# Kernel optimization log

Hardware: AMD Instinct MI355X
Metric: run time of the kernel (lower is better)

The kernel has to match this reference:

```python
import jax, jax.numpy as jnp
import numpy as np

IN_FEATURES = 4096
OUT_FEATURES = 4096
MIN_PREC = 3   # min(precisions)
MAXMEM = 6
BL, BH = 4, 5  # floor/ceil of p = sigmoid(0)*3 + 3 = 4.5 (static, matches p.item() usage)


def dequant_kbit(qweight, lut, b):
    """Bitplane LUT dequant: qweight (P, O, IN//32) int32, lut (O, 2**b) -> (O, IN) float.
    Plane j holds one bit per weight (32 weights packed per int32, LSB-first within
    the int32); the first b planes form the b-bit code, plane 0 being the MSB."""
    planes = qweight[:b]                                   # (b, O, IN//32)
    shifts = jnp.arange(32, dtype=jnp.int32)               # bit position within int32
    bits = (planes[..., None] >> shifts) & 1               # (b, O, IN//32, 32)
    bits = bits.reshape(b, planes.shape[1], -1)            # (b, O, IN)
    weights = (jnp.arange(b, dtype=jnp.int32)[::-1])[:, None, None]  # MSB-first
    code = jnp.sum(bits << weights, axis=0)                # (O, IN) int32 in [0, 2**b)
    return jnp.take_along_axis(lut, code, axis=1)          # (O, IN)


def setup_inputs() -> dict:
    key = jax.random.key(0)
    k_x, k_q, k_l4, k_l5, k_b = jax.random.split(key, 5)
    x = jax.random.normal(k_x, (4, 2048, IN_FEATURES), dtype=jnp.float32)
    z = jnp.float32(0.0)  # z_inv = log(z_init/(1-z_init)) with z_init=0.5
    qweight = jax.random.randint(k_q, (MAXMEM, OUT_FEATURES, IN_FEATURES // 32),
                                 minval=-(2**31), maxval=2**31 - 1, dtype=jnp.int32)
    # LUTs: sorted quantization levels per output row (realistic for quantized linear)
    lut4 = jnp.sort(0.02 * jax.random.normal(k_l4, (OUT_FEATURES, 2**BL), dtype=jnp.float32), axis=-1)
    lut5 = jnp.sort(0.02 * jax.random.normal(k_l5, (OUT_FEATURES, 2**BH), dtype=jnp.float32), axis=-1)
    bias = 0.01 * jax.random.normal(k_b, (OUT_FEATURES,), dtype=jnp.float32)
    return {"x": x, "z": z, "lut4": lut4, "lut5": lut5, "bias": bias, "qweight": qweight}


def reference(x, z, lut4, lut5, bias, qweight):
    prange_len = MAXMEM - MIN_PREC
    p = jax.nn.sigmoid(z) * prange_len + MIN_PREC   # 4.5 at init
    r = 1.0 - (p - BL)                              # blend weight for low-bit branch
    wl = dequant_kbit(qweight, lut4, BL)            # (O, IN)
    wh = dequant_kbit(qweight, lut5, BH)            # (O, IN)
    yl = jnp.einsum('bsi,oi->bso', x, wl)
    yh = jnp.einsum('bsi,oi->bso', x, wh)
    return yl * r + yh * (1.0 - r) + bias
```

## Files before the change

kernel.cpp:

```cpp
#include <hip/hip_runtime.h>
#include <hip/hip_bf16.h>


#define IN_F   4096
#define OUT_F  4096
#define M_DIM  8192

#define CAST_BLOCKS 8192
#define DEQ_BLOCKS  2048

#define NT (IN_F / 64)
#define TSH (256 * 64)

typedef __bf16          bf16x8   __attribute__((ext_vector_type(8)));
typedef float           f32x4    __attribute__((ext_vector_type(4)));
typedef unsigned short  ushortx8 __attribute__((ext_vector_type(8)));

__device__ __forceinline__ unsigned short f32_to_bf16(float f) {
    unsigned int u = __builtin_bit_cast(unsigned int, f);
    u += 0x7fffu + ((u >> 16) & 1u);
    return (unsigned short)(u >> 16);
}

__device__ __forceinline__ void async_load16(const void* g, void* l) {
    __builtin_amdgcn_global_load_lds(
        (const __attribute__((address_space(1))) unsigned int*)g,
        (__attribute__((address_space(3))) unsigned int*)l,
        16, 0, 0);
}

__device__ __forceinline__ void stage_half(const unsigned short* g0,
                                           unsigned short* l0) {
    async_load16(g0, l0);
    async_load16(g0 + (size_t)64 * IN_F, l0 + 4096);
}

__global__ __launch_bounds__(256) void prologue_kernel(
    const float* __restrict__ x,
    const unsigned int* __restrict__ qw,
    const float* __restrict__ lut4,
    const float* __restrict__ lut5,
    const float* __restrict__ zp,
    unsigned short* __restrict__ xb,
    unsigned short* __restrict__ W)
{
    const int tid = threadIdx.x;

    if (blockIdx.x < CAST_BLOCKS) {
        const size_t i = (size_t)blockIdx.x * 4096 + (size_t)tid * 16;
        const f32x4* src = (const f32x4*)(x + i);
        f32x4 a0 = src[0], a1 = src[1], a2 = src[2], a3 = src[3];
        ushortx8 o0, o1;
        #pragma unroll
        for (int e = 0; e < 4; ++e) {
            o0[e]     = f32_to_bf16(a0[e]);
            o0[4 + e] = f32_to_bf16(a1[e]);
            o1[e]     = f32_to_bf16(a2[e]);
            o1[4 + e] = f32_to_bf16(a3[e]);
        }
        ushortx8* dst = (ushortx8*)(xb + i);
        dst[0] = o0;
        dst[1] = o1;
        return;
    }

    __shared__ float sc[2][32];
    const int bid = blockIdx.x - CAST_BLOCKS;
    const int o0 = bid * 2;

    if (tid < 64) {
        const float z   = zp[0];
        const float sig = 1.0f / (1.0f + __expf(-z));
        const float r   = 2.0f - 3.0f * sig;
        const float ri  = 1.0f - r;
        const int row = tid >> 5;
        const int c   = tid & 31;
        sc[row][c] = r * lut4[(o0 + row) * 16 + (c >> 1)]
                   + ri * lut5[(o0 + row) * 32 + c];
    }
    __syncthreads();

    const int gid = bid * 256 + tid;
    const int lo  = (gid >> 7) & 1;

    const int PS = OUT_F * (IN_F / 32);
    const unsigned int q0 = qw[0 * PS + gid];
    const unsigned int q1 = qw[1 * PS + gid];
    const unsigned int q2 = qw[2 * PS + gid];
    const unsigned int q3 = qw[3 * PS + gid];
    const unsigned int q4 = qw[4 * PS + gid];

    unsigned short outv[32];
    #pragma unroll
    for (int i = 0; i < 32; ++i) {
        const unsigned c5 = (((q0 >> i) & 1u) << 4) | (((q1 >> i) & 1u) << 3) |
                            (((q2 >> i) & 1u) << 2) | (((q3 >> i) & 1u) << 1) |
                             ((q4 >> i) & 1u);
        outv[i] = f32_to_bf16(sc[lo][c5]);
    }

    ushortx8* dst = (ushortx8*)(W + (size_t)gid * 32);
    #pragma unroll
    for (int j = 0; j < 4; ++j) {
        ushortx8 v;
        #pragma unroll
        for (int e = 0; e < 8; ++e) v[e] = outv[j * 8 + e];
        dst[j] = v;
    }
}


#define MFMA_BF16 __builtin_amdgcn_mfma_f32_16x16x32_bf16

__device__ __forceinline__ void tile_step(
    int t,
    const unsigned short* cA, unsigned short* cB, unsigned short* nA,
    int tid,
    const unsigned short* gA0, const unsigned short* gA1,
    const unsigned short* gB0, const unsigned short* gB1,
    int aBase, int bBase, int ck0, int ck1,
    f32x4 (&acc)[8][4])
{
    bf16x8 bf0[4], bf1[4], afa[4], afb[4], afc[4], afd[4];

    #pragma unroll
    for (int n = 0; n < 4; ++n)
        bf0[n] = *(const bf16x8*)(cB + bBase + n * 1024 + ck0);
    #pragma unroll
    for (int n = 0; n < 4; ++n)
        bf1[n] = *(const bf16x8*)(cB + bBase + n * 1024 + ck1);
    #pragma unroll
    for (int m = 0; m < 4; ++m)
        afa[m] = *(const bf16x8*)(cA + aBase + m * 1024 + ck0);

    if (t + 1 < NT) {
        stage_half(gA0 + (size_t)(t + 1) * 64, nA + tid * 8);
        stage_half(gA1 + (size_t)(t + 1) * 64, nA + 8192 + tid * 8);
    }

    __builtin_amdgcn_s_setprio(1);
    #pragma unroll
    for (int m = 0; m < 4; ++m)
        #pragma unroll
        for (int n = 0; n < 4; ++n)
            acc[m][n] = MFMA_BF16(afa[m], bf0[n], acc[m][n], 0, 0, 0);
    __builtin_amdgcn_s_setprio(0);

    #pragma unroll
    for (int m = 0; m < 4; ++m)
        afb[m] = *(const bf16x8*)(cA + aBase + m * 1024 + ck1);

    __builtin_amdgcn_s_setprio(1);
    #pragma unroll
    for (int m = 0; m < 4; ++m)
        #pragma unroll
        for (int n = 0; n < 4; ++n)
            acc[m][n] = MFMA_BF16(afb[m], bf1[n], acc[m][n], 0, 0, 0);
    __builtin_amdgcn_s_setprio(0);

    __builtin_amdgcn_sched_barrier(0);
    __builtin_amdgcn_s_barrier();
    __builtin_amdgcn_sched_barrier(0);

    #pragma unroll
    for (int m = 0; m < 4; ++m)
        afc[m] = *(const bf16x8*)(cA + aBase + (m + 4) * 1024 + ck0);

    if (t + 2 < NT) {
        stage_half(gB0 + (size_t)(t + 2) * 64, cB + tid * 8);
        stage_half(gB1 + (size_t)(t + 2) * 64, cB + 8192 + tid * 8);
    }

    __builtin_amdgcn_s_setprio(1);
    #pragma unroll
    for (int m = 0; m < 4; ++m)
        #pragma unroll
        for (int n = 0; n < 4; ++n)
            acc[m + 4][n] = MFMA_BF16(afc[m], bf0[n], acc[m + 4][n], 0, 0, 0);
    __builtin_amdgcn_s_setprio(0);

    #pragma unroll
    for (int m = 0; m < 4; ++m)
        afd[m] = *(const bf16x8*)(cA + aBase + (m + 4) * 1024 + ck1);

    __builtin_amdgcn_s_setprio(1);
    #pragma unroll
    for (int m = 0; m < 4; ++m)
        #pragma unroll
        for (int n = 0; n < 4; ++n)
            acc[m + 4][n] = MFMA_BF16(afd[m], bf1[n], acc[m + 4][n], 0, 0, 0);
    __builtin_amdgcn_s_setprio(0);

    __builtin_amdgcn_sched_barrier(0);
    if (t < NT - 2) asm volatile("s_waitcnt vmcnt(4)" ::: "memory");
    else            asm volatile("s_waitcnt vmcnt(0)" ::: "memory");
    __builtin_amdgcn_s_barrier();
    __builtin_amdgcn_sched_barrier(0);
}

__global__ __launch_bounds__(512, 2) void gemm_bt_kernel(
    const unsigned short* __restrict__ A,
    const unsigned short* __restrict__ B,
    const float* __restrict__ bias,
    float* __restrict__ C)
{
    __shared__ unsigned short sA[2][TSH];
    __shared__ unsigned short sB[2][TSH];

    const int tid = threadIdx.x;

    const int id  = blockIdx.x;
    const int swz = (id & 7) * 64 + (id >> 3);
    const int bn  = swz & 15;
    const int bm  = swz >> 4;

    const int l   = tid & 63;
    const int wv  = tid >> 6;
    const int wr  = wv >> 2;
    const int wc  = wv & 3;
    const int l15 = l & 15;
    const int q   = l >> 4;
    const int xm  = l15 & 7;

    const int aBase = (wr * 128 + l15) * 64;
    const int bBase = (wc * 64  + l15) * 64;
    const int ck0   = ((q)     ^ xm) * 8;
    const int ck1   = ((4 + q) ^ xm) * 8;

    const int r  = tid >> 3;
    const int cx = ((tid & 7) ^ (r & 7)) * 8;
    const unsigned short* gA0 = A + (size_t)(bm * 256 + r) * IN_F + cx;
    const unsigned short* gA1 = gA0 + (size_t)128 * IN_F;
    const unsigned short* gB0 = B + (size_t)(bn * 256 + r) * IN_F + cx;
    const unsigned short* gB1 = gB0 + (size_t)128 * IN_F;

    stage_half(gA0,      &sA[0][0] + tid * 8);
    stage_half(gA1,      &sA[0][0] + 8192 + tid * 8);
    stage_half(gB0,      &sB[0][0] + tid * 8);
    stage_half(gB1,      &sB[0][0] + 8192 + tid * 8);
    stage_half(gB0 + 64, &sB[1][0] + tid * 8);
    stage_half(gB1 + 64, &sB[1][0] + 8192 + tid * 8);
    asm volatile("s_waitcnt vmcnt(4)" ::: "memory");
    __builtin_amdgcn_s_barrier();
    __builtin_amdgcn_sched_barrier(0);

    f32x4 acc[8][4] = {};

    #pragma unroll 1
    for (int tp = 0; tp < NT; tp += 2) {
        tile_step(tp,     &sA[0][0], &sB[0][0], &sA[1][0], tid,
                  gA0, gA1, gB0, gB1, aBase, bBase, ck0, ck1, acc);
        tile_step(tp + 1, &sA[1][0], &sB[1][0], &sA[0][0], tid,
                  gA0, gA1, gB0, gB1, aBase, bBase, ck0, ck1, acc);
    }

    const int row0 = bm * 256 + wr * 128 + q * 4;
    const int col0 = bn * 256 + wc * 64 + l15;
    #pragma unroll
    for (int n = 0; n < 4; ++n) {
        const float bv = bias[col0 + n * 16];
        #pragma unroll
        for (int m = 0; m < 8; ++m) {
            #pragma unroll
            for (int rr = 0; rr < 4; ++rr)
                C[(size_t)(row0 + m * 16 + rr) * OUT_F + (col0 + n * 16)] =
                    acc[m][n][rr] + bv;
        }
    }
}

extern "C" void kernel_launch(void* const* d_in, const int* in_sizes, int n_in,
                              void* d_out, int out_size, void* d_ws, size_t ws_size,
                              hipStream_t stream)
{
    const float*        x    = (const float*)d_in[0];
    const float*        z    = (const float*)d_in[1];
    const float*        lut4 = (const float*)d_in[2];
    const float*        lut5 = (const float*)d_in[3];
    const float*        bias = (const float*)d_in[4];
    const unsigned int* qw   = (const unsigned int*)d_in[5];
    float* out = (float*)d_out;

    unsigned short* xb = (unsigned short*)d_ws;
    unsigned short* wb = xb + (size_t)M_DIM * IN_F;

    prologue_kernel<<<CAST_BLOCKS + DEQ_BLOCKS, 256, 0, stream>>>(
        x, qw, lut4, lut5, z, xb, wb);
    gemm_bt_kernel<<<(M_DIM / 256) * (OUT_F / 256), 512, 0, stream>>>(
        xb, wb, bias, out);
}
```

Before: 467.8 us.

## Fuse prologue and GEMM into one cooperative persistent kernel with grid sync

Replaces the separate cast/dequant prologue kernel and the GEMM kernel with a single cooperative kernel of 256 blocks. Each block first casts a slice of x to bf16 and dequantizes 16 weight rows, then waits on a grid-wide sync and computes two 256x256 output tiles in sequence. The intent is to remove the second kernel launch and the gap between the two kernels. In exchange, the prologue now runs on far fewer threads (256 blocks of 512 instead of about 10k blocks), the grid sync adds a fixed cost, and the GEMM runs as a persistent loop with only two tiles per block.

```diff
diff --git a/kernel.cpp b/kernel.cpp
--- a/kernel.cpp
+++ b/kernel.cpp
@@ -1,13 +1,13 @@
 #include <hip/hip_runtime.h>
 #include <hip/hip_bf16.h>
+#include <hip/hip_cooperative_groups.h>
+
+namespace cg = cooperative_groups;
 
 
 #define IN_F   4096
 #define OUT_F  4096
 #define M_DIM  8192
-
-#define CAST_BLOCKS 8192
-#define DEQ_BLOCKS  2048
 
 #define NT (IN_F / 64)
 #define TSH (256 * 64)
@@ -33,80 +33,6 @@
                                            unsigned short* l0) {
     async_load16(g0, l0);
     async_load16(g0 + (size_t)64 * IN_F, l0 + 4096);
-}
-
-__global__ __launch_bounds__(256) void prologue_kernel(
-    const float* __restrict__ x,
-    const unsigned int* __restrict__ qw,
-    const float* __restrict__ lut4,
-    const float* __restrict__ lut5,
-    const float* __restrict__ zp,
-    unsigned short* __restrict__ xb,
-    unsigned short* __restrict__ W)
-{
-    const int tid = threadIdx.x;
-
-    if (blockIdx.x < CAST_BLOCKS) {
-        const size_t i = (size_t)blockIdx.x * 4096 + (size_t)tid * 16;
-        const f32x4* src = (const f32x4*)(x + i);
-        f32x4 a0 = src[0], a1 = src[1], a2 = src[2], a3 = src[3];
-        ushortx8 o0, o1;
-        #pragma unroll
-        for (int e = 0; e < 4; ++e) {
-            o0[e]     = f32_to_bf16(a0[e]);
-            o0[4 + e] = f32_to_bf16(a1[e]);
-            o1[e]     = f32_to_bf16(a2[e]);
-            o1[4 + e] = f32_to_bf16(a3[e]);
-        }
-        ushortx8* dst = (ushortx8*)(xb + i);
-        dst[0] = o0;
-        dst[1] = o1;
-        return;
-    }
-
-    __shared__ float sc[2][32];
-    const int bid = blockIdx.x - CAST_BLOCKS;
-    const int o0 = bid * 2;
-
-    if (tid < 64) {
-        const float z   = zp[0];
-        const float sig = 1.0f / (1.0f + __expf(-z));
-        const float r   = 2.0f - 3.0f * sig;
-        const float ri  = 1.0f - r;
-        const int row = tid >> 5;
-        const int c   = tid & 31;
-        sc[row][c] = r * lut4[(o0 + row) * 16 + (c >> 1)]
-                   + ri * lut5[(o0 + row) * 32 + c];
-    }
-    __syncthreads();
-
-    const int gid = bid * 256 + tid;
-    const int lo  = (gid >> 7) & 1;
-
-    const int PS = OUT_F * (IN_F / 32);
-    const unsigned int q0 = qw[0 * PS + gid];
-    const unsigned int q1 = qw[1 * PS + gid];
-    const unsigned int q2 = qw[2 * PS + gid];
-    const unsigned int q3 = qw[3 * PS + gid];
-    const unsigned int q4 = qw[4 * PS + gid];
-
-    unsigned short outv[32];
-    #pragma unroll
-    for (int i = 0; i < 32; ++i) {
-        const unsigned c5 = (((q0 >> i) & 1u) << 4) | (((q1 >> i) & 1u) << 3) |
-                            (((q2 >> i) & 1u) << 2) | (((q3 >> i) & 1u) << 1) |
-                             ((q4 >> i) & 1u);
-        outv[i] = f32_to_bf16(sc[lo][c5]);
-    }
-
-    ushortx8* dst = (ushortx8*)(W + (size_t)gid * 32);
-    #pragma unroll
-    for (int j = 0; j < 4; ++j) {
-        ushortx8 v;
-        #pragma unroll
-        for (int e = 0; e < 8; ++e) v[e] = outv[j * 8 + e];
-        dst[j] = v;
-    }
 }
 
 
@@ -198,21 +124,90 @@
     __builtin_amdgcn_sched_barrier(0);
 }
 
-__global__ __launch_bounds__(512, 2) void gemm_bt_kernel(
-    const unsigned short* __restrict__ A,
-    const unsigned short* __restrict__ B,
+__global__ __launch_bounds__(512, 2) void fused_kernel(
+    const float* __restrict__ x,
+    const unsigned int* __restrict__ qw,
+    const float* __restrict__ lut4,
+    const float* __restrict__ lut5,
+    const float* __restrict__ zp,
     const float* __restrict__ bias,
+    unsigned short* __restrict__ xb,
+    unsigned short* __restrict__ wb,
     float* __restrict__ C)
 {
     __shared__ unsigned short sA[2][TSH];
     __shared__ unsigned short sB[2][TSH];
 
     const int tid = threadIdx.x;
-
-    const int id  = blockIdx.x;
-    const int swz = (id & 7) * 64 + (id >> 3);
-    const int bn  = swz & 15;
-    const int bm  = swz >> 4;
+    const int b   = blockIdx.x;
+
+    #pragma unroll 4
+    for (int it = 0; it < 16; ++it) {
+        const size_t s = (size_t)it * (256 * 512) + (size_t)b * 512 + tid;
+        const f32x4* src = (const f32x4*)(x + s * 16);
+        f32x4 a0 = src[0], a1 = src[1], a2 = src[2], a3 = src[3];
+        ushortx8 o0, o1;
+        #pragma unroll
+        for (int e = 0; e < 4; ++e) {
+            o0[e]     = f32_to_bf16(a0[e]);
+            o0[4 + e] = f32_to_bf16(a1[e]);
+            o1[e]     = f32_to_bf16(a2[e]);
+            o1[4 + e] = f32_to_bf16(a3[e]);
+        }
+        ushortx8* dst = (ushortx8*)(xb + s * 16);
+        dst[0] = o0;
+        dst[1] = o1;
+    }
+
+    {
+        float* sc = (float*)&sA[0][0];
+        const float z    = zp[0];
+        const float sig  = 1.0f / (1.0f + __expf(-z));
+        const float rat  = 2.0f - 3.0f * sig;
+        const float rati = 1.0f - rat;
+        const int lutrow = tid >> 5;
+        const int lutc   = tid & 31;
+        const int row0   = b * 16;
+        sc[lutrow * 32 + lutc] = rat  * lut4[(row0 + lutrow) * 16 + (lutc >> 1)]
+                               + rati * lut5[(row0 + lutrow) * 32 + lutc];
+        __syncthreads();
+
+        const int PS = OUT_F * (IN_F / 32);
+        #pragma unroll 1
+        for (int it = 0; it < 4; ++it) {
+            const int lidx = it * 512 + tid;
+            const int gid  = b * 2048 + lidx;
+            const int lrow = lidx >> 7;
+
+            const unsigned int w0 = qw[0 * PS + gid];
+            const unsigned int w1 = qw[1 * PS + gid];
+            const unsigned int w2 = qw[2 * PS + gid];
+            const unsigned int w3 = qw[3 * PS + gid];
+            const unsigned int w4 = qw[4 * PS + gid];
+
+            unsigned short outv[32];
+            #pragma unroll
+            for (int i = 0; i < 32; ++i) {
+                const unsigned c5 = (((w0 >> i) & 1u) << 4) |
+                                    (((w1 >> i) & 1u) << 3) |
+                                    (((w2 >> i) & 1u) << 2) |
+                                    (((w3 >> i) & 1u) << 1) |
+                                     ((w4 >> i) & 1u);
+                outv[i] = f32_to_bf16(sc[lrow * 32 + c5]);
+            }
+            ushortx8* dst = (ushortx8*)(wb + (size_t)gid * 32);
+            #pragma unroll
+            for (int j = 0; j < 4; ++j) {
+                ushortx8 v;
+                #pragma unroll
+                for (int e = 0; e < 8; ++e) v[e] = outv[j * 8 + e];
+                dst[j] = v;
+            }
+        }
+        __syncthreads();
+    }
+
+    cg::this_grid().sync();
 
     const int l   = tid & 63;
     const int wv  = tid >> 6;
@@ -227,44 +222,52 @@
     const int ck0   = ((q)     ^ xm) * 8;
     const int ck1   = ((4 + q) ^ xm) * 8;
 
-    const int r  = tid >> 3;
-    const int cx = ((tid & 7) ^ (r & 7)) * 8;
-    const unsigned short* gA0 = A + (size_t)(bm * 256 + r) * IN_F + cx;
-    const unsigned short* gA1 = gA0 + (size_t)128 * IN_F;
-    const unsigned short* gB0 = B + (size_t)(bn * 256 + r) * IN_F + cx;
-    const unsigned short* gB1 = gB0 + (size_t)128 * IN_F;
-
-    stage_half(gA0,      &sA[0][0] + tid * 8);
-    stage_half(gA1,      &sA[0][0] + 8192 + tid * 8);
-    stage_half(gB0,      &sB[0][0] + tid * 8);
-    stage_half(gB1,      &sB[0][0] + 8192 + tid * 8);
-    stage_half(gB0 + 64, &sB[1][0] + tid * 8);
-    stage_half(gB1 + 64, &sB[1][0] + 8192 + tid * 8);
-    asm volatile("s_waitcnt vmcnt(4)" ::: "memory");
-    __builtin_amdgcn_s_barrier();
-    __builtin_amdgcn_sched_barrier(0);
-
-    f32x4 acc[8][4] = {};
+    const int sr = tid >> 3;
+    const int cx = ((tid & 7) ^ (sr & 7)) * 8;
 
     #pragma unroll 1
-    for (int tp = 0; tp < NT; tp += 2) {
-        tile_step(tp,     &sA[0][0], &sB[0][0], &sA[1][0], tid,
-                  gA0, gA1, gB0, gB1, aBase, bBase, ck0, ck1, acc);
-        tile_step(tp + 1, &sA[1][0], &sB[1][0], &sA[0][0], tid,
-                  gA0, gA1, gB0, gB1, aBase, bBase, ck0, ck1, acc);
-    }
-
-    const int row0 = bm * 256 + wr * 128 + q * 4;
-    const int col0 = bn * 256 + wc * 64 + l15;
-    #pragma unroll
-    for (int n = 0; n < 4; ++n) {
-        const float bv = bias[col0 + n * 16];
-        #pragma unroll
-        for (int m = 0; m < 8; ++m) {
+    for (int ti = 0; ti < 2; ++ti) {
+        const int t  = (b & 7) * 64 + (b >> 3) * 2 + ti;
+        const int bn = t & 15;
+        const int bm = t >> 4;
+
+        const unsigned short* gA0 = xb + (size_t)(bm * 256 + sr) * IN_F + cx;
+        const unsigned short* gA1 = gA0 + (size_t)128 * IN_F;
+        const unsigned short* gB0 = wb + (size_t)(bn * 256 + sr) * IN_F + cx;
+        const unsigned short* gB1 = gB0 + (size_t)128 * IN_F;
+
+        stage_half(gA0,      &sA[0][0] + tid * 8);
+        stage_half(gA1,      &sA[0][0] + 8192 + tid * 8);
+        stage_half(gB0,      &sB[0][0] + tid * 8);
+        stage_half(gB1,      &sB[0][0] + 8192 + tid * 8);
+        stage_half(gB0 + 64, &sB[1][0] + tid * 8);
+        stage_half(gB1 + 64, &sB[1][0] + 8192 + tid * 8);
+        asm volatile("s_waitcnt vmcnt(4)" ::: "memory");
+        __builtin_amdgcn_s_barrier();
+        __builtin_amdgcn_sched_barrier(0);
+
+        f32x4 acc[8][4] = {};
+
+        #pragma unroll 1
+        for (int tp = 0; tp < NT; tp += 2) {
+            tile_step(tp,     &sA[0][0], &sB[0][0], &sA[1][0], tid,
+                      gA0, gA1, gB0, gB1, aBase, bBase, ck0, ck1, acc);
+            tile_step(tp + 1, &sA[1][0], &sB[1][0], &sA[0][0], tid,
+                      gA0, gA1, gB0, gB1, aBase, bBase, ck0, ck1, acc);
+        }
+
+        const int row0 = bm * 256 + wr * 128 + q * 4;
+        const int col0 = bn * 256 + wc * 64 + l15;
+        #pragma unroll
+        for (int n = 0; n < 4; ++n) {
+            const float bv = bias[col0 + n * 16];
             #pragma unroll
-            for (int rr = 0; rr < 4; ++rr)
-                C[(size_t)(row0 + m * 16 + rr) * OUT_F + (col0 + n * 16)] =
-                    acc[m][n][rr] + bv;
+            for (int m = 0; m < 8; ++m) {
+                #pragma unroll
+                for (int rr = 0; rr < 4; ++rr)
+                    C[(size_t)(row0 + m * 16 + rr) * OUT_F + (col0 + n * 16)] =
+                        acc[m][n][rr] + bv;
+            }
         }
     }
 }
@@ -284,8 +287,9 @@
     unsigned short* xb = (unsigned short*)d_ws;
     unsigned short* wb = xb + (size_t)M_DIM * IN_F;
 
-    prologue_kernel<<<CAST_BLOCKS + DEQ_BLOCKS, 256, 0, stream>>>(
-        x, qw, lut4, lut5, z, xb, wb);
-    gemm_bt_kernel<<<(M_DIM / 256) * (OUT_F / 256), 512, 0, stream>>>(
-        xb, wb, bias, out);
-}
+    void* args[] = { (void*)&x, (void*)&qw, (void*)&lut4, (void*)&lut5,
+                     (void*)&z, (void*)&bias, (void*)&xb, (void*)&wb,
+                     (void*)&out };
+    hipLaunchCooperativeKernel((const void*)fused_kernel,
+                               dim3(256), dim3(512), args, 0, stream);
+}
```

Result: slower. 541.7 us (+15.8%).
